# Optimization experiments

Measured on AMD Instinct MI355X. Metric: run time of the kernel, lower is better.

The kernel has to match this reference:

```python
import jax, jax.numpy as jnp
import numpy as np

B, S, HID = 4, 2048, 512
NH, HD = 8, 64          # num heads, head dim (num_kv_heads == NH, so GQA group = 1)
SW = 250                # sliding window
THETA = 10000.0
SCALING = 1.0 / np.sqrt(HD)
NEG_INF = jnp.finfo(jnp.float32).min


def setup_inputs() -> dict:
    key = jax.random.key(0)
    ks = jax.random.split(key, 5)
    w_std = 1.0 / np.sqrt(HID)
    return {
        "hidden_states": jax.random.normal(ks[0], (B, S, HID), jnp.float32),
        "position_ids": jnp.broadcast_to(jnp.arange(S, dtype=jnp.int64), (B, S)),
        "Wq": jax.random.normal(ks[1], (NH * HD, HID), jnp.float32) * w_std,
        "Wk": jax.random.normal(ks[2], (NH * HD, HID), jnp.float32) * w_std,
        "Wv": jax.random.normal(ks[3], (NH * HD, HID), jnp.float32) * w_std,
        "Wo": jax.random.normal(ks[4], (HID, NH * HD), jnp.float32) * w_std,
    }


def _rotate_half(x):
    x1, x2 = jnp.split(x, 2, axis=-1)
    return jnp.concatenate((-x2, x1), axis=-1)


def reference(hidden_states, position_ids, Wq, Wk, Wv, Wo):
    b, s, _ = hidden_states.shape
    dtype = hidden_states.dtype

    # QKV projections (Linear: x @ W.T, no bias) -> [b, h, s, d]
    q = (hidden_states @ Wq.T).reshape(b, s, NH, HD).transpose(0, 2, 1, 3)
    k = (hidden_states @ Wk.T).reshape(b, s, NH, HD).transpose(0, 2, 1, 3)
    v = (hidden_states @ Wv.T).reshape(b, s, NH, HD).transpose(0, 2, 1, 3)

    # Rotary embedding (MimiRotaryEmbedding), computed in fp32
    inv_freq = 1.0 / (THETA ** (jnp.arange(0, HD, 2, dtype=jnp.float32) / HD))
    freqs = position_ids.astype(jnp.float32)[:, :, None] * inv_freq[None, None, :]  # [b, s, HD/2]
    emb = jnp.concatenate((freqs, freqs), axis=-1)                                   # [b, s, HD]
    cos = jnp.cos(emb).astype(dtype)[:, None, :, :]  # unsqueeze head dim
    sin = jnp.sin(emb).astype(dtype)[:, None, :, :]
    q = q * cos + _rotate_half(q) * sin
    k = k * cos + _rotate_half(k) * sin

    # Sliding-window causal additive mask: keep kv iff q_idx >= kv_idx and q_idx - kv_idx <= SW
    idx = jnp.arange(s)
    keep = (idx[:, None] >= idx[None, :]) & ((idx[:, None] - idx[None, :]) <= SW)
    bias = jnp.where(keep, 0.0, NEG_INF).astype(jnp.float32)  # [s, s]

    # Eager attention: full scores, fp32 softmax (num_key_value_groups == 1)
    scores = jnp.einsum("bhqd,bhkd->bhqk", q, k) * SCALING
    scores = scores.astype(jnp.float32) + bias[None, None, :, :]
    attn = jax.nn.softmax(scores, axis=-1).astype(dtype)
    out = jnp.einsum("bhqk,bhkd->bhqd", attn, v)

    # merge heads and output projection
    out = out.transpose(0, 2, 1, 3).reshape(b, s, NH * HD)
    return out @ Wo.T
```

## Files before the change

### kernel.cpp

```cpp
#include <hip/hip_runtime.h>
#include <hip/hip_bf16.h>
#include <math.h>


#define B_   4
#define S_   2048
#define HID_ 512
#define NH_  8
#define HD_  64
#define SW_  250

typedef __bf16 bf16x8 __attribute__((ext_vector_type(8)));
typedef float f32x4 __attribute__((ext_vector_type(4)));
using bf16_t = __hip_bfloat16;
typedef unsigned int u32;

__device__ __forceinline__ void glds16(const bf16_t* g, bf16_t* l) {
    __builtin_amdgcn_global_load_lds(
        (const __attribute__((address_space(1))) u32*)g,
        (__attribute__((address_space(3))) u32*)l, 16, 0, 0);
}

__global__ __launch_bounds__(256) void cvt_all(
    const float* __restrict__ X,  const float* __restrict__ Wq,
    const float* __restrict__ Wk, const float* __restrict__ Wv,
    const float* __restrict__ Wo,
    bf16_t* __restrict__ Xb, bf16_t* __restrict__ Wcat, bf16_t* __restrict__ Wob)
{
    const int blk = blockIdx.x;
    const float* s; bf16_t* d; size_t base;
    if (blk < 2048)      { s = X;  d = Xb;            base = (size_t)blk * 2048; }
    else if (blk < 2176) { s = Wq; d = Wcat;          base = (size_t)(blk - 2048) * 2048; }
    else if (blk < 2304) { s = Wk; d = Wcat + 262144; base = (size_t)(blk - 2176) * 2048; }
    else if (blk < 2432) { s = Wv; d = Wcat + 524288; base = (size_t)(blk - 2304) * 2048; }
    else                 { s = Wo; d = Wob;           base = (size_t)(blk - 2432) * 2048; }
    size_t i = base + (size_t)threadIdx.x * 8;
    float4 a = *reinterpret_cast<const float4*>(s + i);
    float4 b = *reinterpret_cast<const float4*>(s + i + 4);
    bf16x8 r;
    r[0] = (__bf16)a.x; r[1] = (__bf16)a.y; r[2] = (__bf16)a.z; r[3] = (__bf16)a.w;
    r[4] = (__bf16)b.x; r[5] = (__bf16)b.y; r[6] = (__bf16)b.z; r[7] = (__bf16)b.w;
    *reinterpret_cast<bf16x8*>(d + i) = r;
}

__global__ __launch_bounds__(256) void qkv_gemm(
    const bf16_t* __restrict__ Xb, const bf16_t* __restrict__ Wcat,
    bf16_t* __restrict__ Q, bf16_t* __restrict__ Kbuf, bf16_t* __restrict__ Vt)
{
    __shared__ __align__(16) bf16_t As[128 * 32];
    __shared__ __align__(16) bf16_t Bs[128 * 32];
    const int tid = threadIdx.x;
    const int wave = tid >> 6, lane = tid & 63;
    const int quad = lane >> 4, l16 = lane & 15;
    const int wm = wave & 1, wn = wave >> 1;
    const int m0 = blockIdx.x * 128, n0 = blockIdx.y * 128;

    f32x4 acc[4][4] = {};
    for (int k0 = 0; k0 < HID_; k0 += 32) {
#pragma unroll
        for (int t = 0; t < 2; ++t) {
            int flat = t * 2048 + tid * 8;
            int row = flat >> 5, col = flat & 31;
            glds16(Xb + (size_t)(m0 + row) * HID_ + k0 + col, As + flat);
            glds16(Wcat + (size_t)(n0 + row) * HID_ + k0 + col, Bs + flat);
        }
        __syncthreads();
        bf16x8 af[4], bfr[4];
#pragma unroll
        for (int i = 0; i < 4; ++i) {
            af[i]  = *reinterpret_cast<const bf16x8*>(&As[(wm * 64 + i * 16 + l16) * 32 + quad * 8]);
            bfr[i] = *reinterpret_cast<const bf16x8*>(&Bs[(wn * 64 + i * 16 + l16) * 32 + quad * 8]);
        }
#pragma unroll
        for (int mi = 0; mi < 4; ++mi)
#pragma unroll
            for (int ni = 0; ni < 4; ++ni)
                acc[mi][ni] = __builtin_amdgcn_mfma_f32_16x16x32_bf16(af[mi], bfr[ni], acc[mi][ni], 0, 0, 0);
        __syncthreads();
    }

    const int seg = n0 >> 9;
    const int npr = n0 & 511;
    const int hh  = (npr + wn * 64) >> 6;

    if (seg < 2) {
        bf16_t* Y = (seg == 0) ? Q : Kbuf;
        const float qs = (seg == 0) ? 0.125f : 1.0f;
        const float c = 0.41524101186f;
        float inv0 = exp2f(-(float)l16 * c);
        float inv1 = exp2f(-(float)(l16 + 16) * c);
#pragma unroll
        for (int mi = 0; mi < 4; ++mi)
#pragma unroll
            for (int r = 0; r < 4; ++r) {
                int m = m0 + wm * 64 + mi * 16 + quad * 4 + r;
                int bb = m >> 11, s = m & (S_ - 1);
                size_t base = ((size_t)(bb * NH_ + hh) * S_ + s) * HD_;
#pragma unroll
                for (int ip = 0; ip < 2; ++ip) {
                    float inv = ip ? inv1 : inv0;
                    float sn, cs_;
                    sincosf((float)s * inv, &sn, &cs_);
                    int d = ip * 16 + l16;
                    float x1 = acc[mi][ip][r], x2 = acc[mi][ip + 2][r];
                    Y[base + d]      = __float2bfloat16((x1 * cs_ - x2 * sn) * qs);
                    Y[base + d + 32] = __float2bfloat16((x2 * cs_ + x1 * sn) * qs);
                }
            }
    } else {
#pragma unroll
        for (int mi = 0; mi < 4; ++mi)
#pragma unroll
            for (int r = 0; r < 4; ++r) {
                int m = m0 + wm * 64 + mi * 16 + quad * 4 + r;
                int bb = m >> 11, s = m & (S_ - 1);
                size_t vb = ((size_t)(bb * NH_ + hh) * HD_) * S_ + s;
#pragma unroll
                for (int ni = 0; ni < 4; ++ni) {
                    int d = ni * 16 + l16;
                    Vt[vb + (size_t)d * S_] = __float2bfloat16(acc[mi][ni][r]);
                }
            }
    }
}

__global__ __launch_bounds__(256) void attn_mfma(
    const bf16_t* __restrict__ Q, const bf16_t* __restrict__ K,
    const bf16_t* __restrict__ Vt, bf16_t* __restrict__ A)
{
    __shared__ __align__(16) __bf16 pt[4][16][296];
    const int wave = threadIdx.x >> 6, lane = threadIdx.x & 63;
    const int quad = lane >> 4, l16 = lane & 15;
    const int h = blockIdx.y, b = blockIdx.z;
    const int q0 = (blockIdx.x * 4 + wave) * 16;
    const size_t bh  = (size_t)(b * NH_ + h) * S_;
    const size_t bhd = (size_t)(b * NH_ + h) * HD_;

    bf16x8 qf0, qf1;
    {
        const bf16_t* qp = Q + (bh + q0 + l16) * HD_ + quad * 8;
        qf0 = *reinterpret_cast<const bf16x8*>(qp);
        qf1 = *reinterpret_cast<const bf16x8*>(qp + 32);
    }

    const int kstart = (q0 > SW_) ? ((q0 - SW_) & ~31) : 0;
    const int kend   = q0 + 15;
    const int nt     = (kend - kstart + 32) >> 5;

    f32x4 s[9][2];
#pragma unroll
    for (int t = 0; t < 9; ++t) {
        if (t < nt) {
            const int kb = kstart + t * 32;
#pragma unroll
            for (int half = 0; half < 2; ++half) {
                const bf16_t* kp = K + (bh + kb + half * 16 + l16) * HD_ + quad * 8;
                bf16x8 k0 = *reinterpret_cast<const bf16x8*>(kp);
                bf16x8 k1 = *reinterpret_cast<const bf16x8*>(kp + 32);
                f32x4 z = {};
                z = __builtin_amdgcn_mfma_f32_16x16x32_bf16(qf0, k0, z, 0, 0, 0);
                z = __builtin_amdgcn_mfma_f32_16x16x32_bf16(qf1, k1, z, 0, 0, 0);
                const int key = kb + half * 16 + l16;
#pragma unroll
                for (int r = 0; r < 4; ++r) {
                    int qq = q0 + quad * 4 + r;
                    bool keep = (key <= qq) && (qq - key <= SW_);
                    s[t][half][r] = keep ? z[r] : -3.0e38f;
                }
            }
        }
    }

    float mx[4] = {-3.0e38f, -3.0e38f, -3.0e38f, -3.0e38f};
#pragma unroll
    for (int t = 0; t < 9; ++t)
        if (t < nt)
#pragma unroll
            for (int half = 0; half < 2; ++half)
#pragma unroll
                for (int r = 0; r < 4; ++r)
                    mx[r] = fmaxf(mx[r], s[t][half][r]);
#pragma unroll
    for (int off = 1; off < 16; off <<= 1)
#pragma unroll
        for (int r = 0; r < 4; ++r)
            mx[r] = fmaxf(mx[r], __shfl_xor(mx[r], off, 64));

    float sum[4] = {0.f, 0.f, 0.f, 0.f};
#pragma unroll
    for (int t = 0; t < 9; ++t)
        if (t < nt)
#pragma unroll
            for (int half = 0; half < 2; ++half)
#pragma unroll
                for (int r = 0; r < 4; ++r) {
                    float p = __expf(s[t][half][r] - mx[r]);
                    sum[r] += p;
                    pt[wave][quad * 4 + r][t * 32 + half * 16 + l16] = (__bf16)p;
                }
#pragma unroll
    for (int off = 1; off < 16; off <<= 1)
#pragma unroll
        for (int r = 0; r < 4; ++r)
            sum[r] += __shfl_xor(sum[r], off, 64);

    f32x4 o[4] = {};
#pragma unroll
    for (int t = 0; t < 9; ++t) {
        if (t < nt) {
            const int kb = kstart + t * 32;
            bf16x8 pf = *reinterpret_cast<const bf16x8*>(&pt[wave][l16][t * 32 + quad * 8]);
#pragma unroll
            for (int nf = 0; nf < 4; ++nf) {
                const bf16_t* vp = Vt + (bhd + nf * 16 + l16) * S_ + kb + quad * 8;
                bf16x8 vf = *reinterpret_cast<const bf16x8*>(vp);
                o[nf] = __builtin_amdgcn_mfma_f32_16x16x32_bf16(pf, vf, o[nf], 0, 0, 0);
            }
        }
    }

    float inv_l[4];
#pragma unroll
    for (int r = 0; r < 4; ++r) inv_l[r] = 1.0f / sum[r];
#pragma unroll
    for (int nf = 0; nf < 4; ++nf)
#pragma unroll
        for (int r = 0; r < 4; ++r) {
            int qq = q0 + quad * 4 + r;
            A[((size_t)(b * S_ + qq)) * HID_ + h * HD_ + nf * 16 + l16] =
                __float2bfloat16(o[nf][r] * inv_l[r]);
        }
}

__global__ __launch_bounds__(256) void out_proj(
    const bf16_t* __restrict__ Ain, const bf16_t* __restrict__ Wob,
    float* __restrict__ out)
{
    __shared__ __align__(16) bf16_t As[128 * 32];
    __shared__ __align__(16) bf16_t Bs[64 * 32];
    const int tid = threadIdx.x;
    const int wave = tid >> 6, lane = tid & 63;
    const int quad = lane >> 4, l16 = lane & 15;
    const int m0 = blockIdx.x * 128, n0 = blockIdx.y * 64;

    f32x4 acc[2][4] = {};
    for (int k0 = 0; k0 < HID_; k0 += 32) {
#pragma unroll
        for (int t = 0; t < 2; ++t) {
            int flat = t * 2048 + tid * 8;
            int row = flat >> 5, col = flat & 31;
            glds16(Ain + (size_t)(m0 + row) * HID_ + k0 + col, As + flat);
        }
        {
            int flat = tid * 8;
            int row = flat >> 5, col = flat & 31;
            glds16(Wob + (size_t)(n0 + row) * HID_ + k0 + col, Bs + flat);
        }
        __syncthreads();
        bf16x8 af[2], bfr[4];
#pragma unroll
        for (int i = 0; i < 2; ++i)
            af[i] = *reinterpret_cast<const bf16x8*>(&As[(wave * 32 + i * 16 + l16) * 32 + quad * 8]);
#pragma unroll
        for (int i = 0; i < 4; ++i)
            bfr[i] = *reinterpret_cast<const bf16x8*>(&Bs[(i * 16 + l16) * 32 + quad * 8]);
#pragma unroll
        for (int mi = 0; mi < 2; ++mi)
#pragma unroll
            for (int ni = 0; ni < 4; ++ni)
                acc[mi][ni] = __builtin_amdgcn_mfma_f32_16x16x32_bf16(af[mi], bfr[ni], acc[mi][ni], 0, 0, 0);
        __syncthreads();
    }
#pragma unroll
    for (int mi = 0; mi < 2; ++mi)
#pragma unroll
        for (int ni = 0; ni < 4; ++ni)
#pragma unroll
            for (int r = 0; r < 4; ++r) {
                int m = m0 + wave * 32 + mi * 16 + quad * 4 + r;
                int n = n0 + ni * 16 + l16;
                out[(size_t)m * HID_ + n] = acc[mi][ni][r];
            }
}

extern "C" void kernel_launch(void* const* d_in, const int* in_sizes, int n_in,
                              void* d_out, int out_size, void* d_ws, size_t ws_size,
                              hipStream_t stream)
{
    const float* X  = (const float*)d_in[0];
    const float* Wq = (const float*)d_in[2];
    const float* Wk = (const float*)d_in[3];
    const float* Wv = (const float*)d_in[4];
    const float* Wo = (const float*)d_in[5];

    char* ws = (char*)d_ws;
    const size_t elems = (size_t)B_ * NH_ * S_ * HD_;
    const size_t wsz   = (size_t)HID_ * HID_;
    bf16_t* Q    = (bf16_t*)ws;
    bf16_t* K    = Q + elems;
    bf16_t* Vt   = K + elems;
    bf16_t* Xb   = Vt + elems;
    bf16_t* A    = Xb;
    bf16_t* Wcat = Xb + elems;
    bf16_t* Wob  = Wcat + 3 * wsz;

    cvt_all<<<2560, 256, 0, stream>>>(X, Wq, Wk, Wv, Wo, Xb, Wcat, Wob);
    qkv_gemm<<<dim3(64, 12), 256, 0, stream>>>(Xb, Wcat, Q, K, Vt);
    attn_mfma<<<dim3(32, 8, 4), 256, 0, stream>>>(Q, K, Vt, A);
    out_proj<<<dim3(64, 8), 256, 0, stream>>>(A, Wob, (float*)d_out);
}
```

Before: 155.4 us.

## Stage QKV epilogue through LDS, precompute RoPE table, transpose attention score MFMA

```diff
diff --git a/kernel.cpp b/kernel.cpp
--- a/kernel.cpp
+++ b/kernel.cpp
@@ -11,6 +11,7 @@
 #define SW_  250
 
 typedef __bf16 bf16x8 __attribute__((ext_vector_type(8)));
+typedef __bf16 bf16x4 __attribute__((ext_vector_type(4)));
 typedef float f32x4 __attribute__((ext_vector_type(4)));
 using bf16_t = __hip_bfloat16;
 typedef unsigned int u32;
@@ -25,9 +26,23 @@
     const float* __restrict__ X,  const float* __restrict__ Wq,
     const float* __restrict__ Wk, const float* __restrict__ Wv,
     const float* __restrict__ Wo,
-    bf16_t* __restrict__ Xb, bf16_t* __restrict__ Wcat, bf16_t* __restrict__ Wob)
+    bf16_t* __restrict__ Xb, bf16_t* __restrict__ Wcat, bf16_t* __restrict__ Wob,
+    float2* __restrict__ rope)
 {
     const int blk = blockIdx.x;
+    if (blk >= 2560) {
+        int e0 = ((blk - 2560) * 256 + threadIdx.x) * 4;
+#pragma unroll
+        for (int j = 0; j < 4; ++j) {
+            int e = e0 + j;
+            int s = e >> 5, i = e & 31;
+            float inv = exp2f(-(float)i * 0.41524101186f);
+            float sn, cs;
+            sincosf((float)s * inv, &sn, &cs);
+            rope[e] = make_float2(cs, sn);
+        }
+        return;
+    }
     const float* s; bf16_t* d; size_t base;
     if (blk < 2048)      { s = X;  d = Xb;            base = (size_t)blk * 2048; }
     else if (blk < 2176) { s = Wq; d = Wcat;          base = (size_t)(blk - 2048) * 2048; }
@@ -45,10 +60,12 @@
 
 __global__ __launch_bounds__(256) void qkv_gemm(
     const bf16_t* __restrict__ Xb, const bf16_t* __restrict__ Wcat,
+    const float2* __restrict__ rope,
     bf16_t* __restrict__ Q, bf16_t* __restrict__ Kbuf, bf16_t* __restrict__ Vt)
 {
-    __shared__ __align__(16) bf16_t As[128 * 32];
-    __shared__ __align__(16) bf16_t Bs[128 * 32];
+    __shared__ __align__(16) bf16_t smem[4 * 64 * 68];
+    bf16_t* As = smem;
+    bf16_t* Bs = smem + 4096;
     const int tid = threadIdx.x;
     const int wave = tid >> 6, lane = tid & 63;
     const int quad = lane >> 4, l16 = lane & 15;
@@ -78,49 +95,56 @@
                 acc[mi][ni] = __builtin_amdgcn_mfma_f32_16x16x32_bf16(af[mi], bfr[ni], acc[mi][ni], 0, 0, 0);
         __syncthreads();
     }
-
     const int seg = n0 >> 9;
     const int npr = n0 & 511;
     const int hh  = (npr + wn * 64) >> 6;
+    bf16_t* wt = smem + wave * (64 * 68);
+    const int mbase = m0 + wm * 64;
+    const int bb = mbase >> 11;
+    const int sbase = mbase & (S_ - 1);
 
     if (seg < 2) {
+        const float qs = (seg == 0) ? 0.125f : 1.0f;
+#pragma unroll
+        for (int mi = 0; mi < 4; ++mi)
+#pragma unroll
+            for (int r = 0; r < 4; ++r) {
+                int lrow = mi * 16 + quad * 4 + r;
+                int s = sbase + lrow;
+#pragma unroll
+                for (int ip = 0; ip < 2; ++ip) {
+                    float2 t2 = rope[(size_t)s * 32 + ip * 16 + l16];
+                    float x1 = acc[mi][ip][r], x2 = acc[mi][ip + 2][r];
+                    wt[lrow * 68 + ip * 16 + l16]      = __float2bfloat16((x1 * t2.x - x2 * t2.y) * qs);
+                    wt[lrow * 68 + ip * 16 + l16 + 32] = __float2bfloat16((x2 * t2.x + x1 * t2.y) * qs);
+                }
+            }
         bf16_t* Y = (seg == 0) ? Q : Kbuf;
-        const float qs = (seg == 0) ? 0.125f : 1.0f;
-        const float c = 0.41524101186f;
-        float inv0 = exp2f(-(float)l16 * c);
-        float inv1 = exp2f(-(float)(l16 + 16) * c);
+#pragma unroll
+        for (int it = 0; it < 8; ++it) {
+            int e = it * 64 + lane;
+            int sr = e >> 3, doff = (e & 7) * 8;
+            size_t g = ((size_t)(bb * NH_ + hh) * S_ + sbase + sr) * HD_ + doff;
+            *reinterpret_cast<bf16x8*>(Y + g) =
+                *reinterpret_cast<const bf16x8*>(wt + sr * 68 + doff);
+        }
+    } else {
 #pragma unroll
         for (int mi = 0; mi < 4; ++mi)
 #pragma unroll
-            for (int r = 0; r < 4; ++r) {
-                int m = m0 + wm * 64 + mi * 16 + quad * 4 + r;
-                int bb = m >> 11, s = m & (S_ - 1);
-                size_t base = ((size_t)(bb * NH_ + hh) * S_ + s) * HD_;
-#pragma unroll
-                for (int ip = 0; ip < 2; ++ip) {
-                    float inv = ip ? inv1 : inv0;
-                    float sn, cs_;
-                    sincosf((float)s * inv, &sn, &cs_);
-                    int d = ip * 16 + l16;
-                    float x1 = acc[mi][ip][r], x2 = acc[mi][ip + 2][r];
-                    Y[base + d]      = __float2bfloat16((x1 * cs_ - x2 * sn) * qs);
-                    Y[base + d + 32] = __float2bfloat16((x2 * cs_ + x1 * sn) * qs);
-                }
-            }
-    } else {
-#pragma unroll
-        for (int mi = 0; mi < 4; ++mi)
-#pragma unroll
-            for (int r = 0; r < 4; ++r) {
-                int m = m0 + wm * 64 + mi * 16 + quad * 4 + r;
-                int bb = m >> 11, s = m & (S_ - 1);
-                size_t vb = ((size_t)(bb * NH_ + hh) * HD_) * S_ + s;
-#pragma unroll
-                for (int ni = 0; ni < 4; ++ni) {
-                    int d = ni * 16 + l16;
-                    Vt[vb + (size_t)d * S_] = __float2bfloat16(acc[mi][ni][r]);
-                }
-            }
+            for (int ni = 0; ni < 4; ++ni)
+#pragma unroll
+                for (int r = 0; r < 4; ++r)
+                    wt[(ni * 16 + l16) * 68 + mi * 16 + quad * 4 + r] =
+                        __float2bfloat16(acc[mi][ni][r]);
+#pragma unroll
+        for (int it = 0; it < 8; ++it) {
+            int e = it * 64 + lane;
+            int d = e >> 3, soff = (e & 7) * 8;
+            size_t g = ((size_t)(bb * NH_ + hh) * HD_ + d) * S_ + sbase + soff;
+            *reinterpret_cast<bf16x8*>(Vt + g) =
+                *reinterpret_cast<const bf16x8*>(wt + d * 68 + soff);
+        }
     }
 }
 
@@ -129,6 +153,7 @@
     const bf16_t* __restrict__ Vt, bf16_t* __restrict__ A)
 {
     __shared__ __align__(16) __bf16 pt[4][16][296];
+    __shared__ float sums_l[4][16];
     const int wave = threadIdx.x >> 6, lane = threadIdx.x & 63;
     const int quad = lane >> 4, l16 = lane & 15;
     const int h = blockIdx.y, b = blockIdx.z;
@@ -144,8 +169,8 @@
     }
 
     const int kstart = (q0 > SW_) ? ((q0 - SW_) & ~31) : 0;
-    const int kend   = q0 + 15;
-    const int nt     = (kend - kstart + 32) >> 5;
+    const int nt = (q0 + 15 - kstart + 32) >> 5;
+    const int qq = q0 + l16;
 
     f32x4 s[9][2];
 #pragma unroll
@@ -158,12 +183,12 @@
                 bf16x8 k0 = *reinterpret_cast<const bf16x8*>(kp);
                 bf16x8 k1 = *reinterpret_cast<const bf16x8*>(kp + 32);
                 f32x4 z = {};
-                z = __builtin_amdgcn_mfma_f32_16x16x32_bf16(qf0, k0, z, 0, 0, 0);
-                z = __builtin_amdgcn_mfma_f32_16x16x32_bf16(qf1, k1, z, 0, 0, 0);
-                const int key = kb + half * 16 + l16;
+                z = __builtin_amdgcn_mfma_f32_16x16x32_bf16(k0, qf0, z, 0, 0, 0);
+                z = __builtin_amdgcn_mfma_f32_16x16x32_bf16(k1, qf1, z, 0, 0, 0);
+                const int kbase = kb + half * 16 + quad * 4;
 #pragma unroll
                 for (int r = 0; r < 4; ++r) {
-                    int qq = q0 + quad * 4 + r;
+                    int key = kbase + r;
                     bool keep = (key <= qq) && (qq - key <= SW_);
                     s[t][half][r] = keep ? z[r] : -3.0e38f;
                 }
@@ -171,7 +196,7 @@
         }
     }
 
-    float mx[4] = {-3.0e38f, -3.0e38f, -3.0e38f, -3.0e38f};
+    float mx = -3.0e38f;
 #pragma unroll
     for (int t = 0; t < 9; ++t)
         if (t < nt)
@@ -179,30 +204,28 @@
             for (int half = 0; half < 2; ++half)
 #pragma unroll
                 for (int r = 0; r < 4; ++r)
-                    mx[r] = fmaxf(mx[r], s[t][half][r]);
-#pragma unroll
-    for (int off = 1; off < 16; off <<= 1)
-#pragma unroll
-        for (int r = 0; r < 4; ++r)
-            mx[r] = fmaxf(mx[r], __shfl_xor(mx[r], off, 64));
-
-    float sum[4] = {0.f, 0.f, 0.f, 0.f};
+                    mx = fmaxf(mx, s[t][half][r]);
+    mx = fmaxf(mx, __shfl_xor(mx, 16, 64));
+    mx = fmaxf(mx, __shfl_xor(mx, 32, 64));
+
+    float sum = 0.f;
 #pragma unroll
     for (int t = 0; t < 9; ++t)
         if (t < nt)
 #pragma unroll
-            for (int half = 0; half < 2; ++half)
+            for (int half = 0; half < 2; ++half) {
+                bf16x4 pk;
 #pragma unroll
                 for (int r = 0; r < 4; ++r) {
-                    float p = __expf(s[t][half][r] - mx[r]);
-                    sum[r] += p;
-                    pt[wave][quad * 4 + r][t * 32 + half * 16 + l16] = (__bf16)p;
+                    float p = __expf(s[t][half][r] - mx);
+                    sum += p;
+                    pk[r] = (__bf16)p;
                 }
-#pragma unroll
-    for (int off = 1; off < 16; off <<= 1)
-#pragma unroll
-        for (int r = 0; r < 4; ++r)
-            sum[r] += __shfl_xor(sum[r], off, 64);
+                *reinterpret_cast<bf16x4*>(&pt[wave][l16][t * 32 + half * 16 + quad * 4]) = pk;
+            }
+    sum += __shfl_xor(sum, 16, 64);
+    sum += __shfl_xor(sum, 32, 64);
+    if (quad == 0) sums_l[wave][l16] = sum;
 
     f32x4 o[4] = {};
 #pragma unroll
@@ -221,13 +244,13 @@
 
     float inv_l[4];
 #pragma unroll
-    for (int r = 0; r < 4; ++r) inv_l[r] = 1.0f / sum[r];
+    for (int r = 0; r < 4; ++r) inv_l[r] = 1.0f / sums_l[wave][quad * 4 + r];
 #pragma unroll
     for (int nf = 0; nf < 4; ++nf)
 #pragma unroll
         for (int r = 0; r < 4; ++r) {
-            int qq = q0 + quad * 4 + r;
-            A[((size_t)(b * S_ + qq)) * HID_ + h * HD_ + nf * 16 + l16] =
+            int qr = q0 + quad * 4 + r;
+            A[((size_t)(b * S_ + qr)) * HID_ + h * HD_ + nf * 16 + l16] =
                 __float2bfloat16(o[nf][r] * inv_l[r]);
         }
 }
@@ -303,9 +326,10 @@
     bf16_t* A    = Xb;
     bf16_t* Wcat = Xb + elems;
     bf16_t* Wob  = Wcat + 3 * wsz;
-
-    cvt_all<<<2560, 256, 0, stream>>>(X, Wq, Wk, Wv, Wo, Xb, Wcat, Wob);
-    qkv_gemm<<<dim3(64, 12), 256, 0, stream>>>(Xb, Wcat, Q, K, Vt);
+    float2* rope = (float2*)(Wob + wsz);
+
+    cvt_all<<<2624, 256, 0, stream>>>(X, Wq, Wk, Wv, Wo, Xb, Wcat, Wob, rope);
+    qkv_gemm<<<dim3(64, 12), 256, 0, stream>>>(Xb, Wcat, rope, Q, K, Vt);
     attn_mfma<<<dim3(32, 8, 4), 256, 0, stream>>>(Q, K, Vt, A);
     out_proj<<<dim3(64, 8), 256, 0, stream>>>(A, Wob, (float*)d_out);
 }
```

Measured after the change: 146.9 us. -5.5%, faster.
